# Kernel tuning notes

Hardware: AMD Instinct MI355X
Metric: run time of the kernel (lower is better)

Reference implementation:

```python
import jax, jax.numpy as jnp
import numpy as np

B, T, H, W, C = 4, 8, 64, 64, 256
WS = (2, 8, 8)        # window size (t,h,w); T,H,W chosen divisible -> no padding path
SS = (1, 4, 4)        # shift = window//2 (use_shift=True)
NH = 8
HD = C // NH
HID = int(C * 2.0)    # mlp_ratio=2.0
N = WS[0] * WS[1] * WS[2]          # 128 tokens per window
SCALE = HD ** -0.5
RPB_SIZE = (2 * WS[0] - 1) * (2 * WS[1] - 1) * (2 * WS[2] - 1)  # 675


def _rel_index(ws):
    coords = np.stack(np.meshgrid(np.arange(ws[0]), np.arange(ws[1]), np.arange(ws[2]), indexing='ij'))
    cf = coords.reshape(3, -1)
    rc = (cf[:, :, None] - cf[:, None, :]).transpose(1, 2, 0).astype(np.int64)
    rc[..., 0] += ws[0] - 1
    rc[..., 1] += ws[1] - 1
    rc[..., 2] += ws[2] - 1
    rc[..., 0] *= (2 * ws[1] - 1) * (2 * ws[2] - 1)
    rc[..., 1] *= 2 * ws[2] - 1
    return rc.sum(-1)  # [N, N]

REL_IDX = jnp.asarray(_rel_index(WS))


def _attn_mask(t, h, w, ws, ss):
    img = np.zeros((t, h, w), np.float32)
    cnt = 0
    for ts in (slice(0, -ws[0]), slice(-ws[0], -ss[0]), slice(-ss[0], None)):
        for hs in (slice(0, -ws[1]), slice(-ws[1], -ss[1]), slice(-ss[1], None)):
            for wsl in (slice(0, -ws[2]), slice(-ws[2], -ss[2]), slice(-ss[2], None)):
                img[ts, hs, wsl] = cnt
                cnt += 1
    mw = img.reshape(t // ws[0], ws[0], h // ws[1], ws[1], w // ws[2], ws[2])
    mw = mw.transpose(0, 2, 4, 1, 3, 5).reshape(-1, ws[0] * ws[1] * ws[2])  # [nW, N]
    am = mw[:, None, :] - mw[:, :, None]
    return np.where(am != 0, -100.0, 0.0).astype(np.float32)  # [nW, N, N]

ATTN_MASK = jnp.asarray(_attn_mask(T, H, W, WS, SS))


def layernorm(x, g, b):
    m = x.mean(-1, keepdims=True)
    v = x.var(-1, keepdims=True)
    return (x - m) / jnp.sqrt(v + 1e-5) * g + b


def win_part(x):
    # [B,T,H,W,C] -> [B*nW, N, C]
    x = x.reshape(B, T // WS[0], WS[0], H // WS[1], WS[1], W // WS[2], WS[2], C)
    return x.transpose(0, 1, 3, 5, 2, 4, 6, 7).reshape(-1, N, C)


def win_rev(w):
    x = w.reshape(B, T // WS[0], H // WS[1], W // WS[2], WS[0], WS[1], WS[2], C)
    return x.transpose(0, 1, 4, 2, 5, 3, 6, 7).reshape(B, T, H, W, C)


def win_attn(xw, rpb, qkv_w, qkv_b, proj_w, proj_b, mask):
    Bw = xw.shape[0]
    qkv = (xw @ qkv_w + qkv_b).reshape(Bw, N, 3, NH, HD).transpose(2, 0, 3, 1, 4)
    q, k, v = qkv[0] * SCALE, qkv[1], qkv[2]          # [Bw, NH, N, HD]
    a = jnp.einsum('bhnd,bhmd->bhnm', q, k)
    bias = rpb[REL_IDX.reshape(-1)].reshape(N, N, NH).transpose(2, 0, 1)
    a = a + bias[None]
    if mask is not None:
        nW = mask.shape[0]
        a = (a.reshape(Bw // nW, nW, NH, N, N) + mask[None, :, None]).reshape(Bw, NH, N, N)
    a = jax.nn.softmax(a, -1)
    o = jnp.einsum('bhnm,bhmd->bhnd', a, v).transpose(0, 2, 1, 3).reshape(Bw, N, C)
    return o @ proj_w + proj_b


def mlp(x, w1, b1, w2, b2):
    return jax.nn.gelu(x @ w1 + b1, approximate=False) @ w2 + b2


def setup_inputs():
    key = jax.random.key(0)
    ks = jax.random.split(key, 16)
    s = 0.02
    inp = {
        'x': jax.random.normal(ks[0], (B, T, H, W, C), jnp.float32),
        'rpb1': jax.random.normal(ks[1], (RPB_SIZE, NH), jnp.float32) * s,
        'qkv_w1': jax.random.normal(ks[2], (C, 3 * C), jnp.float32) * s,
        'qkv_b1': jnp.zeros((3 * C,), jnp.float32),
        'proj_w1': jax.random.normal(ks[3], (C, C), jnp.float32) * s,
        'proj_b1': jnp.zeros((C,), jnp.float32),
        'rpb2': jax.random.normal(ks[4], (RPB_SIZE, NH), jnp.float32) * s,
        'qkv_w2': jax.random.normal(ks[5], (C, 3 * C), jnp.float32) * s,
        'qkv_b2': jnp.zeros((3 * C,), jnp.float32),
        'proj_w2': jax.random.normal(ks[6], (C, C), jnp.float32) * s,
        'proj_b2': jnp.zeros((C,), jnp.float32),
        'g1': jnp.ones((C,), jnp.float32), 'be1': jnp.zeros((C,), jnp.float32),
        'g2': jnp.ones((C,), jnp.float32), 'be2': jnp.zeros((C,), jnp.float32),
        'g3': jnp.ones((C,), jnp.float32), 'be3': jnp.zeros((C,), jnp.float32),
        'g4': jnp.ones((C,), jnp.float32), 'be4': jnp.zeros((C,), jnp.float32),
        'm1w1': jax.random.normal(ks[7], (C, HID), jnp.float32) * s,
        'm1b1': jnp.zeros((HID,), jnp.float32),
        'm1w2': jax.random.normal(ks[8], (HID, C), jnp.float32) * s,
        'm1b2': jnp.zeros((C,), jnp.float32),
        'm2w1': jax.random.normal(ks[9], (C, HID), jnp.float32) * s,
        'm2b1': jnp.zeros((HID,), jnp.float32),
        'm2w2': jax.random.normal(ks[10], (HID, C), jnp.float32) * s,
        'm2b2': jnp.zeros((C,), jnp.float32),
    }
    return inp


def reference(x, rpb1, qkv_w1, qkv_b1, proj_w1, proj_b1,
              rpb2, qkv_w2, qkv_b2, proj_w2, proj_b2,
              g1, be1, g2, be2, g3, be3, g4, be4,
              m1w1, m1b1, m1w2, m1b2, m2w1, m2b1, m2w2, m2b2):
    # block 1: plain window attention (no shift)
    shortcut = x
    xw = win_part(layernorm(x, g1, be1))
    aw = win_attn(xw, rpb1, qkv_w1, qkv_b1, proj_w1, proj_b1, None)
    x = shortcut + win_rev(aw)
    x = x + mlp(layernorm(x, g2, be2), m1w1, m1b1, m1w2, m1b2)
    # block 2: shifted window attention with mask
    shortcut = x
    xn = layernorm(x, g3, be3)
    sx = jnp.roll(xn, (-SS[0], -SS[1], -SS[2]), axis=(1, 2, 3))
    aw = win_attn(win_part(sx), rpb2, qkv_w2, qkv_b2, proj_w2, proj_b2, ATTN_MASK)
    x = shortcut + jnp.roll(win_rev(aw), SS, axis=(1, 2, 3))
    x = x + mlp(layernorm(x, g4, be4), m2w1, m2b1, m2w2, m2b2)
    return x
```

## Files before the change

kernel.cpp:

```cpp
#include <hip/hip_runtime.h>
#include <stdint.h>

typedef __bf16 bf16_t;
using bf16x8 = __attribute__((ext_vector_type(8))) __bf16;
using f32x4  = __attribute__((ext_vector_type(4))) float;

#define DEVINL __device__ __forceinline__

DEVINL void gload_lds16(const bf16_t* g, char* l) {
  __builtin_amdgcn_global_load_lds(
      (const __attribute__((address_space(1))) void*)g,
      (__attribute__((address_space(3))) void*)l, 16, 0, 0);
}

__global__ void conv_w(const float* __restrict__ w, bf16_t* __restrict__ wt,
                       int kshift, int N, int total) {
  int i = blockIdx.x * 256 + threadIdx.x;
  if (i >= total) return;
  int n = i >> kshift, k = i & ((1 << kshift) - 1);
  wt[i] = (bf16_t)w[(size_t)k * N + n];
}

__global__ void build_bias(const float* __restrict__ rpb, float* __restrict__ tab) {
  int idx = blockIdx.x * 256 + threadIdx.x;
  int n = idx >> 7, m = idx & 127;
  int it1 = n >> 6, ih1 = (n >> 3) & 7, iw1 = n & 7;
  int it2 = m >> 6, ih2 = (m >> 3) & 7, iw2 = m & 7;
  int ridx = (it1 - it2 + 1) * 225 + (ih1 - ih2 + 7) * 15 + (iw1 - iw2 + 7);
#pragma unroll
  for (int h = 0; h < 8; ++h)
    tab[(h << 14) + idx] = rpb[ridx * 8 + h];
}

__global__ __launch_bounds__(256)
void ln_kernel(const float* __restrict__ x, const float* __restrict__ g,
               const float* __restrict__ b, bf16_t* __restrict__ out) {
  int row = blockIdx.x * 4 + (threadIdx.x >> 6);
  int lane = threadIdx.x & 63;
  float4 v = *((const float4*)(x + (size_t)row * 256) + lane);
  float s = v.x + v.y + v.z + v.w;
#pragma unroll
  for (int m = 1; m < 64; m <<= 1) s += __shfl_xor(s, m);
  float mean = s * 0.00390625f;
  float dx = v.x - mean, dy = v.y - mean, dz = v.z - mean, dw = v.w - mean;
  float s2 = dx * dx + dy * dy + dz * dz + dw * dw;
#pragma unroll
  for (int m = 1; m < 64; m <<= 1) s2 += __shfl_xor(s2, m);
  float rstd = rsqrtf(s2 * 0.00390625f + 1e-5f);
  float4 gv = *((const float4*)g + lane);
  float4 bv = *((const float4*)b + lane);
  union { bf16_t h[4]; uint2 u; } pk;
  pk.h[0] = (bf16_t)(dx * rstd * gv.x + bv.x);
  pk.h[1] = (bf16_t)(dy * rstd * gv.y + bv.y);
  pk.h[2] = (bf16_t)(dz * rstd * gv.z + bv.z);
  pk.h[3] = (bf16_t)(dw * rstd * gv.w + bv.w);
  *(uint2*)(out + (size_t)row * 256 + lane * 4) = pk.u;
}

template <int EPI>
__global__ __launch_bounds__(256, 2)
void gemm_bt(const bf16_t* __restrict__ A, const bf16_t* __restrict__ Bt,
             const float* __restrict__ bias, const float* __restrict__ resid,
             void* __restrict__ outp, int M, int N, int K, float qscale, int qcols) {
  __shared__ __align__(16) char ldsA[16384];
  __shared__ __align__(16) char ldsB[16384];
  const int tid = threadIdx.x;
  const int lane = tid & 63, wid = tid >> 6;
  const int l15 = lane & 15, l4 = lane >> 4;
  const int tn = blockIdx.x, tm = blockIdx.y;
  const int wm = wid >> 1, wn = wid & 1;

  f32x4 acc[4][4] = {};
  const int nK = K >> 6;
  const size_t arow0 = (size_t)(tm * 128) * K;

  for (int kt = 0; kt < nK; ++kt) {
    const int kb = kt * 64;
#pragma unroll
    for (int i = 0; i < 4; ++i) {
      int c = i * 256 + tid;
      int row = c >> 3, slot = c & 7;
      int ss = slot ^ (row & 7);
      gload_lds16(A + arow0 + (size_t)row * K + kb + ss * 8,
                  ldsA + (i * 256 + wid * 64) * 16);
      gload_lds16(Bt + (size_t)(tn * 128 + row) * K + kb + ss * 8,
                  ldsB + (i * 256 + wid * 64) * 16);
    }
    __syncthreads();
    bf16x8 af[4][2], bfr[4][2];
#pragma unroll
    for (int mi = 0; mi < 4; ++mi) {
      int row = wm * 64 + mi * 16 + l15;
      int sw = (row & 7) << 4;
#pragma unroll
      for (int kk = 0; kk < 2; ++kk)
        af[mi][kk] = *(const bf16x8*)(ldsA + row * 128 + ((kk * 64 + l4 * 16) ^ sw));
    }
#pragma unroll
    for (int ni = 0; ni < 4; ++ni) {
      int row = wn * 64 + ni * 16 + l15;
      int sw = (row & 7) << 4;
#pragma unroll
      for (int kk = 0; kk < 2; ++kk)
        bfr[ni][kk] = *(const bf16x8*)(ldsB + row * 128 + ((kk * 64 + l4 * 16) ^ sw));
    }
#pragma unroll
    for (int kk = 0; kk < 2; ++kk)
#pragma unroll
      for (int mi = 0; mi < 4; ++mi)
#pragma unroll
        for (int ni = 0; ni < 4; ++ni)
          acc[mi][ni] = __builtin_amdgcn_mfma_f32_16x16x32_bf16(
              af[mi][kk], bfr[ni][kk], acc[mi][ni], 0, 0, 0);
    __syncthreads();
  }

#pragma unroll
  for (int mi = 0; mi < 4; ++mi) {
#pragma unroll
    for (int ni = 0; ni < 4; ++ni) {
      int col = tn * 128 + wn * 64 + ni * 16 + l15;
      float bv = bias[col];
#pragma unroll
      for (int v = 0; v < 4; ++v) {
        int row = tm * 128 + wm * 64 + mi * 16 + l4 * 4 + v;
        float val = acc[mi][ni][v] + bv;
        size_t idx = (size_t)row * N + col;
        if constexpr (EPI == 0) {
          if (col < qcols) val *= qscale;
          ((bf16_t*)outp)[idx] = (bf16_t)val;
        } else if constexpr (EPI == 1) {
          ((float*)outp)[idx] = resid[idx] + val;
        } else {
          ((bf16_t*)outp)[idx] =
              (bf16_t)(0.5f * val * (1.0f + erff(val * 0.7071067811865475f)));
        }
      }
    }
  }
}

template <bool SHIFTED>
__global__ __launch_bounds__(256, 2)
void attn_kernel(const bf16_t* __restrict__ qkv, const float* __restrict__ btab,
                 bf16_t* __restrict__ o) {
  __shared__ int tok_s[128];
  __shared__ int rid_s[128];
  __shared__ __align__(16) char VtL[8192];
  __shared__ __align__(16) char PL[32768];

  const int tid = threadIdx.x, lane = tid & 63, wid = tid >> 6;
  const int l15 = lane & 15, l4 = lane >> 4;
  const int blk = blockIdx.x;
  const int head = blk & 7;
  const int win = blk >> 3;
  const int b = win >> 8, rem = win & 255;
  const int tw = rem >> 6, hw = (rem >> 3) & 7, ww = rem & 7;

  if (tid < 128) {
    int it = tid >> 6, ih = (tid >> 3) & 7, iw = tid & 7;
    int pt = tw * 2 + it, ph = hw * 8 + ih, pw = ww * 8 + iw;
    int t = pt, h = ph, w = pw;
    if (SHIFTED) {
      t = (pt + 1) & 7; h = (ph + 4) & 63; w = (pw + 4) & 63;
      int rt = pt < 6 ? 0 : (pt < 7 ? 1 : 2);
      int rh = ph < 56 ? 0 : (ph < 60 ? 1 : 2);
      int rw2 = pw < 56 ? 0 : (pw < 60 ? 1 : 2);
      rid_s[tid] = rt * 9 + rh * 3 + rw2;
    }
    tok_s[tid] = ((b * 8 + t) << 12) + (h << 6) + w;
  }
  __syncthreads();

  const int hoff = head << 5;
#pragma unroll
  for (int i = 0; i < 2; ++i) {
    int c = i * 256 + tid;
    int tok = c >> 2, dc = c & 3;
    bf16x8 vv = *(const bf16x8*)(qkv + (size_t)tok_s[tok] * 768 + 512 + hoff + dc * 8);
#pragma unroll
    for (int j = 0; j < 8; ++j) {
      int d = dc * 8 + j;
      *(bf16_t*)(VtL + d * 256 + ((tok * 2) ^ ((d & 7) << 4))) = vv[j];
    }
  }

  bf16x8 qf[2], kf[8];
#pragma unroll
  for (int mi = 0; mi < 2; ++mi) {
    int tok = tok_s[wid * 32 + mi * 16 + l15];
    qf[mi] = *(const bf16x8*)(qkv + (size_t)tok * 768 + hoff + l4 * 8);
  }
#pragma unroll
  for (int ni = 0; ni < 8; ++ni) {
    int tok = tok_s[ni * 16 + l15];
    kf[ni] = *(const bf16x8*)(qkv + (size_t)tok * 768 + 256 + hoff + l4 * 8);
  }
  const f32x4 zz = {0.f, 0.f, 0.f, 0.f};
  f32x4 s[2][8];
#pragma unroll
  for (int mi = 0; mi < 2; ++mi)
#pragma unroll
    for (int ni = 0; ni < 8; ++ni)
      s[mi][ni] = __builtin_amdgcn_mfma_f32_16x16x32_bf16(qf[mi], kf[ni], zz, 0, 0, 0);

  const float* bt = btab + (head << 14);
#pragma unroll
  for (int mi = 0; mi < 2; ++mi) {
#pragma unroll
    for (int v = 0; v < 4; ++v) {
      int row = wid * 32 + mi * 16 + l4 * 4 + v;
      float mx = -1e30f;
#pragma unroll
      for (int ni = 0; ni < 8; ++ni) {
        int col = ni * 16 + l15;
        float xx = s[mi][ni][v] + bt[(row << 7) + col];
        if (SHIFTED) { if (rid_s[row] != rid_s[col]) xx -= 100.f; }
        s[mi][ni][v] = xx;
        mx = fmaxf(mx, xx);
      }
#pragma unroll
      for (int d = 1; d < 16; d <<= 1) mx = fmaxf(mx, __shfl_xor(mx, d));
      float sum = 0.f;
#pragma unroll
      for (int ni = 0; ni < 8; ++ni) {
        float e = __expf(s[mi][ni][v] - mx);
        s[mi][ni][v] = e;
        sum += e;
      }
#pragma unroll
      for (int d = 1; d < 16; d <<= 1) sum += __shfl_xor(sum, d);
      float inv = 1.0f / sum;
      int sw = (row & 7) << 4;
#pragma unroll
      for (int ni = 0; ni < 8; ++ni) {
        int col = ni * 16 + l15;
        *(bf16_t*)(PL + row * 256 + ((col * 2) ^ sw)) = (bf16_t)(s[mi][ni][v] * inv);
      }
    }
  }
  __syncthreads();

  f32x4 oacc[2][2] = {};
#pragma unroll
  for (int kk = 0; kk < 4; ++kk) {
    bf16x8 pf[2], vf[2];
#pragma unroll
    for (int mi = 0; mi < 2; ++mi) {
      int row = wid * 32 + mi * 16 + l15;
      pf[mi] = *(const bf16x8*)(PL + row * 256 + ((kk * 64 + l4 * 16) ^ ((row & 7) << 4)));
    }
#pragma unroll
    for (int nj = 0; nj < 2; ++nj) {
      int d = nj * 16 + l15;
      vf[nj] = *(const bf16x8*)(VtL + d * 256 + ((kk * 64 + l4 * 16) ^ ((d & 7) << 4)));
    }
#pragma unroll
    for (int mi = 0; mi < 2; ++mi)
#pragma unroll
      for (int nj = 0; nj < 2; ++nj)
        oacc[mi][nj] = __builtin_amdgcn_mfma_f32_16x16x32_bf16(pf[mi], vf[nj], oacc[mi][nj], 0, 0, 0);
  }
#pragma unroll
  for (int mi = 0; mi < 2; ++mi)
#pragma unroll
    for (int v = 0; v < 4; ++v) {
      int tok = tok_s[wid * 32 + mi * 16 + l4 * 4 + v];
#pragma unroll
      for (int nj = 0; nj < 2; ++nj) {
        int col = nj * 16 + l15;
        o[(size_t)tok * 256 + hoff + col] = (bf16_t)(oacc[mi][nj][v]);
      }
    }
}

extern "C" void kernel_launch(void* const* d_in, const int* in_sizes, int n_in,
                              void* d_out, int out_size, void* d_ws, size_t ws_size,
                              hipStream_t stream) {
  const float* x       = (const float*)d_in[0];
  const float* rpb1    = (const float*)d_in[1];
  const float* qkv_w1  = (const float*)d_in[2];
  const float* qkv_b1  = (const float*)d_in[3];
  const float* proj_w1 = (const float*)d_in[4];
  const float* proj_b1 = (const float*)d_in[5];
  const float* rpb2    = (const float*)d_in[6];
  const float* qkv_w2  = (const float*)d_in[7];
  const float* qkv_b2  = (const float*)d_in[8];
  const float* proj_w2 = (const float*)d_in[9];
  const float* proj_b2 = (const float*)d_in[10];
  const float* g1  = (const float*)d_in[11];
  const float* be1 = (const float*)d_in[12];
  const float* g2  = (const float*)d_in[13];
  const float* be2 = (const float*)d_in[14];
  const float* g3  = (const float*)d_in[15];
  const float* be3 = (const float*)d_in[16];
  const float* g4  = (const float*)d_in[17];
  const float* be4 = (const float*)d_in[18];
  const float* m1w1 = (const float*)d_in[19];
  const float* m1b1 = (const float*)d_in[20];
  const float* m1w2 = (const float*)d_in[21];
  const float* m1b2 = (const float*)d_in[22];
  const float* m2w1 = (const float*)d_in[23];
  const float* m2b1 = (const float*)d_in[24];
  const float* m2w2 = (const float*)d_in[25];
  const float* m2b2 = (const float*)d_in[26];
  float* out = (float*)d_out;

  char* ws = (char*)d_ws;
  bf16_t* qkvb = (bf16_t*)ws;
  bf16_t* xn   = (bf16_t*)(ws + 201326592ull);
  bf16_t* wts  = (bf16_t*)(ws + 268435456ull);
  float* btab1 = (float*)(ws + 270532608ull);
  float* btab2 = btab1 + 131072;

  bf16_t* qw1t = wts;
  bf16_t* pw1t = wts + 196608;
  bf16_t* a1t  = wts + 262144;
  bf16_t* a2t  = wts + 393216;
  bf16_t* qw2t = wts + 524288;
  bf16_t* pw2t = wts + 720896;
  bf16_t* c1t  = wts + 786432;
  bf16_t* c2t  = wts + 917504;

  conv_w<<<768, 256, 0, stream>>>(qkv_w1, qw1t, 8, 768, 196608);
  conv_w<<<256, 256, 0, stream>>>(proj_w1, pw1t, 8, 256, 65536);
  conv_w<<<512, 256, 0, stream>>>(m1w1, a1t, 8, 512, 131072);
  conv_w<<<512, 256, 0, stream>>>(m1w2, a2t, 9, 256, 131072);
  conv_w<<<768, 256, 0, stream>>>(qkv_w2, qw2t, 8, 768, 196608);
  conv_w<<<256, 256, 0, stream>>>(proj_w2, pw2t, 8, 256, 65536);
  conv_w<<<512, 256, 0, stream>>>(m2w1, c1t, 8, 512, 131072);
  conv_w<<<512, 256, 0, stream>>>(m2w2, c2t, 9, 256, 131072);
  build_bias<<<64, 256, 0, stream>>>(rpb1, btab1);
  build_bias<<<64, 256, 0, stream>>>(rpb2, btab2);

  const float SC = 0.17677669529663687f;
  const int M = 131072;

  ln_kernel<<<32768, 256, 0, stream>>>(x, g1, be1, xn);
  gemm_bt<0><<<dim3(6, 1024), 256, 0, stream>>>(xn, qw1t, qkv_b1, nullptr, qkvb, M, 768, 256, SC, 256);
  attn_kernel<false><<<8192, 256, 0, stream>>>(qkvb, btab1, xn);
  gemm_bt<1><<<dim3(2, 1024), 256, 0, stream>>>(xn, pw1t, proj_b1, x, out, M, 256, 256, 1.f, 0);
  ln_kernel<<<32768, 256, 0, stream>>>(out, g2, be2, xn);
  gemm_bt<2><<<dim3(4, 1024), 256, 0, stream>>>(xn, a1t, m1b1, nullptr, qkvb, M, 512, 256, 1.f, 0);
  gemm_bt<1><<<dim3(2, 1024), 256, 0, stream>>>(qkvb, a2t, m1b2, out, out, M, 256, 512, 1.f, 0);

  ln_kernel<<<32768, 256, 0, stream>>>(out, g3, be3, xn);
  gemm_bt<0><<<dim3(6, 1024), 256, 0, stream>>>(xn, qw2t, qkv_b2, nullptr, qkvb, M, 768, 256, SC, 256);
  attn_kernel<true><<<8192, 256, 0, stream>>>(qkvb, btab2, xn);
  gemm_bt<1><<<dim3(2, 1024), 256, 0, stream>>>(xn, pw2t, proj_b2, out, out, M, 256, 256, 1.f, 0);
  ln_kernel<<<32768, 256, 0, stream>>>(out, g4, be4, xn);
  gemm_bt<2><<<dim3(4, 1024), 256, 0, stream>>>(xn, c1t, m2b1, nullptr, qkvb, M, 512, 256, 1.f, 0);
  gemm_bt<1><<<dim3(2, 1024), 256, 0, stream>>>(qkvb, c2t, m2b2, out, out, M, 256, 512, 1.f, 0);
}
```

Baseline: 1.256 ms.

## Transpose attention score MFMA, fold bias+mask into bf16 accumulator init

Rewrites the attention kernel to compute S^T (K as A operand, Q as B), which puts each query's scores in one lane column. Row max/sum then need only two cross-lane shuffles, and P and O can be written with packed 8-byte stores. The relative position bias is precomputed in bf16, with the shifted-window mask folded into 8 per-category tables, and loaded directly as the MFMA accumulator init. This removes the per-element bias add and mask compare. Occupancy hint is raised to 3 blocks per SM; bias is rounded to bf16, a small precision change.

```diff
diff --git a/kernel.cpp b/kernel.cpp
--- a/kernel.cpp
+++ b/kernel.cpp
@@ -11,6 +11,13 @@
   __builtin_amdgcn_global_load_lds(
       (const __attribute__((address_space(1))) void*)g,
       (__attribute__((address_space(3))) void*)l, 16, 0, 0);
+}
+
+DEVINL uint2 pack4(float a, float b, float c, float d) {
+  union { bf16_t h[4]; uint2 u; } pk;
+  pk.h[0] = (bf16_t)a; pk.h[1] = (bf16_t)b;
+  pk.h[2] = (bf16_t)c; pk.h[3] = (bf16_t)d;
+  return pk.u;
 }
 
 __global__ void conv_w(const float* __restrict__ w, bf16_t* __restrict__ wt,
@@ -21,7 +28,7 @@
   wt[i] = (bf16_t)w[(size_t)k * N + n];
 }
 
-__global__ void build_bias(const float* __restrict__ rpb, float* __restrict__ tab) {
+__global__ void build_bias1(const float* __restrict__ rpb, bf16_t* __restrict__ tab) {
   int idx = blockIdx.x * 256 + threadIdx.x;
   int n = idx >> 7, m = idx & 127;
   int it1 = n >> 6, ih1 = (n >> 3) & 7, iw1 = n & 7;
@@ -29,7 +36,27 @@
   int ridx = (it1 - it2 + 1) * 225 + (ih1 - ih2 + 7) * 15 + (iw1 - iw2 + 7);
 #pragma unroll
   for (int h = 0; h < 8; ++h)
-    tab[(h << 14) + idx] = rpb[ridx * 8 + h];
+    tab[(h << 14) + idx] = (bf16_t)rpb[ridx * 8 + h];
+}
+
+__global__ void build_bias2(const float* __restrict__ rpb, bf16_t* __restrict__ tab) {
+  int idx = blockIdx.x * 256 + threadIdx.x;
+  int cat = blockIdx.y;
+  int ct = cat >> 2, ch = (cat >> 1) & 1, cw = cat & 1;
+  int n = idx >> 7, m = idx & 127;
+  int it1 = n >> 6, ih1 = (n >> 3) & 7, iw1 = n & 7;
+  int it2 = m >> 6, ih2 = (m >> 3) & 7, iw2 = m & 7;
+  int rt1 = ct ? (it1 == 0 ? 1 : 2) : 0;
+  int rh1 = ch ? (ih1 < 4 ? 1 : 2) : 0;
+  int rw1 = cw ? (iw1 < 4 ? 1 : 2) : 0;
+  int rt2 = ct ? (it2 == 0 ? 1 : 2) : 0;
+  int rh2 = ch ? (ih2 < 4 ? 1 : 2) : 0;
+  int rw2 = cw ? (iw2 < 4 ? 1 : 2) : 0;
+  float msk = (rt1 != rt2 || rh1 != rh2 || rw1 != rw2) ? -100.f : 0.f;
+  int ridx = (it1 - it2 + 1) * 225 + (ih1 - ih2 + 7) * 15 + (iw1 - iw2 + 7);
+#pragma unroll
+  for (int h = 0; h < 8; ++h)
+    tab[(size_t)((cat * 8 + h) << 14) + idx] = (bf16_t)(rpb[ridx * 8 + h] + msk);
 }
 
 __global__ __launch_bounds__(256)
@@ -141,13 +168,12 @@
 }
 
 template <bool SHIFTED>
-__global__ __launch_bounds__(256, 2)
-void attn_kernel(const bf16_t* __restrict__ qkv, const float* __restrict__ btab,
+__global__ __launch_bounds__(256, 3)
+void attn_kernel(const bf16_t* __restrict__ qkv, const bf16_t* __restrict__ btab,
                  bf16_t* __restrict__ o) {
   __shared__ int tok_s[128];
-  __shared__ int rid_s[128];
   __shared__ __align__(16) char VtL[8192];
-  __shared__ __align__(16) char PL[32768];
+  __shared__ __align__(16) char PLt[32768];
 
   const int tid = threadIdx.x, lane = tid & 63, wid = tid >> 6;
   const int l15 = lane & 15, l4 = lane >> 4;
@@ -163,14 +189,18 @@
     int t = pt, h = ph, w = pw;
     if (SHIFTED) {
       t = (pt + 1) & 7; h = (ph + 4) & 63; w = (pw + 4) & 63;
-      int rt = pt < 6 ? 0 : (pt < 7 ? 1 : 2);
-      int rh = ph < 56 ? 0 : (ph < 60 ? 1 : 2);
-      int rw2 = pw < 56 ? 0 : (pw < 60 ? 1 : 2);
-      rid_s[tid] = rt * 9 + rh * 3 + rw2;
     }
     tok_s[tid] = ((b * 8 + t) << 12) + (h << 6) + w;
   }
   __syncthreads();
+
+  const bf16_t* bt;
+  if (SHIFTED) {
+    int cat = ((tw == 3) ? 4 : 0) | ((hw == 7) ? 2 : 0) | ((ww == 7) ? 1 : 0);
+    bt = btab + ((size_t)(cat * 8 + head) << 14);
+  } else {
+    bt = btab + ((size_t)head << 14);
+  }
 
   const int hoff = head << 5;
 #pragma unroll
@@ -185,58 +215,61 @@
     }
   }
 
-  bf16x8 qf[2], kf[8];
-#pragma unroll
-  for (int mi = 0; mi < 2; ++mi) {
-    int tok = tok_s[wid * 32 + mi * 16 + l15];
-    qf[mi] = *(const bf16x8*)(qkv + (size_t)tok * 768 + hoff + l4 * 8);
-  }
-#pragma unroll
-  for (int ni = 0; ni < 8; ++ni) {
-    int tok = tok_s[ni * 16 + l15];
-    kf[ni] = *(const bf16x8*)(qkv + (size_t)tok * 768 + 256 + hoff + l4 * 8);
-  }
-  const f32x4 zz = {0.f, 0.f, 0.f, 0.f};
-  f32x4 s[2][8];
-#pragma unroll
-  for (int mi = 0; mi < 2; ++mi)
-#pragma unroll
-    for (int ni = 0; ni < 8; ++ni)
-      s[mi][ni] = __builtin_amdgcn_mfma_f32_16x16x32_bf16(qf[mi], kf[ni], zz, 0, 0, 0);
-
-  const float* bt = btab + (head << 14);
-#pragma unroll
-  for (int mi = 0; mi < 2; ++mi) {
-#pragma unroll
-    for (int v = 0; v < 4; ++v) {
-      int row = wid * 32 + mi * 16 + l4 * 4 + v;
-      float mx = -1e30f;
-#pragma unroll
-      for (int ni = 0; ni < 8; ++ni) {
-        int col = ni * 16 + l15;
-        float xx = s[mi][ni][v] + bt[(row << 7) + col];
-        if (SHIFTED) { if (rid_s[row] != rid_s[col]) xx -= 100.f; }
-        s[mi][ni][v] = xx;
-        mx = fmaxf(mx, xx);
-      }
-#pragma unroll
-      for (int d = 1; d < 16; d <<= 1) mx = fmaxf(mx, __shfl_xor(mx, d));
-      float sum = 0.f;
-#pragma unroll
-      for (int ni = 0; ni < 8; ++ni) {
-        float e = __expf(s[mi][ni][v] - mx);
-        s[mi][ni][v] = e;
+  bf16x8 kf[8], qf[2];
+#pragma unroll
+  for (int ki = 0; ki < 8; ++ki) {
+    int tok = tok_s[ki * 16 + l15];
+    kf[ki] = *(const bf16x8*)(qkv + (size_t)tok * 768 + 256 + hoff + l4 * 8);
+  }
+#pragma unroll
+  for (int qi = 0; qi < 2; ++qi) {
+    int tok = tok_s[wid * 32 + qi * 16 + l15];
+    qf[qi] = *(const bf16x8*)(qkv + (size_t)tok * 768 + hoff + l4 * 8);
+  }
+
+  f32x4 st[8][2];
+#pragma unroll
+  for (int ki = 0; ki < 8; ++ki)
+#pragma unroll
+    for (int qi = 0; qi < 2; ++qi) {
+      int q = wid * 32 + qi * 16 + l15;
+      uint2 bu = *(const uint2*)(bt + (q << 7) + ki * 16 + l4 * 4);
+      f32x4 c;
+      c[0] = __uint_as_float(bu.x << 16);
+      c[1] = __uint_as_float(bu.x & 0xffff0000u);
+      c[2] = __uint_as_float(bu.y << 16);
+      c[3] = __uint_as_float(bu.y & 0xffff0000u);
+      st[ki][qi] = __builtin_amdgcn_mfma_f32_16x16x32_bf16(kf[ki], qf[qi], c, 0, 0, 0);
+    }
+
+#pragma unroll
+  for (int qi = 0; qi < 2; ++qi) {
+    float mx = -1e30f;
+#pragma unroll
+    for (int ki = 0; ki < 8; ++ki)
+#pragma unroll
+      for (int v = 0; v < 4; ++v) mx = fmaxf(mx, st[ki][qi][v]);
+    mx = fmaxf(mx, __shfl_xor(mx, 16));
+    mx = fmaxf(mx, __shfl_xor(mx, 32));
+    float sum = 0.f;
+#pragma unroll
+    for (int ki = 0; ki < 8; ++ki)
+#pragma unroll
+      for (int v = 0; v < 4; ++v) {
+        float e = __expf(st[ki][qi][v] - mx);
+        st[ki][qi][v] = e;
         sum += e;
       }
-#pragma unroll
-      for (int d = 1; d < 16; d <<= 1) sum += __shfl_xor(sum, d);
-      float inv = 1.0f / sum;
-      int sw = (row & 7) << 4;
-#pragma unroll
-      for (int ni = 0; ni < 8; ++ni) {
-        int col = ni * 16 + l15;
-        *(bf16_t*)(PL + row * 256 + ((col * 2) ^ sw)) = (bf16_t)(s[mi][ni][v] * inv);
-      }
+    sum += __shfl_xor(sum, 16);
+    sum += __shfl_xor(sum, 32);
+    float inv = 1.0f / sum;
+    int q = wid * 32 + qi * 16 + l15;
+    int sw = (q & 7) << 5;
+#pragma unroll
+    for (int ki = 0; ki < 8; ++ki) {
+      uint2 pk = pack4(st[ki][qi][0] * inv, st[ki][qi][1] * inv,
+                       st[ki][qi][2] * inv, st[ki][qi][3] * inv);
+      *(uint2*)(PLt + q * 256 + ((ki * 32 + l4 * 8) ^ sw)) = pk;
     }
   }
   __syncthreads();
@@ -244,34 +277,34 @@
   f32x4 oacc[2][2] = {};
 #pragma unroll
   for (int kk = 0; kk < 4; ++kk) {
-    bf16x8 pf[2], vf[2];
-#pragma unroll
-    for (int mi = 0; mi < 2; ++mi) {
-      int row = wid * 32 + mi * 16 + l15;
-      pf[mi] = *(const bf16x8*)(PL + row * 256 + ((kk * 64 + l4 * 16) ^ ((row & 7) << 4)));
-    }
-#pragma unroll
-    for (int nj = 0; nj < 2; ++nj) {
-      int d = nj * 16 + l15;
-      vf[nj] = *(const bf16x8*)(VtL + d * 256 + ((kk * 64 + l4 * 16) ^ ((d & 7) << 4)));
-    }
-#pragma unroll
-    for (int mi = 0; mi < 2; ++mi)
-#pragma unroll
-      for (int nj = 0; nj < 2; ++nj)
-        oacc[mi][nj] = __builtin_amdgcn_mfma_f32_16x16x32_bf16(pf[mi], vf[nj], oacc[mi][nj], 0, 0, 0);
-  }
-#pragma unroll
-  for (int mi = 0; mi < 2; ++mi)
-#pragma unroll
-    for (int v = 0; v < 4; ++v) {
-      int tok = tok_s[wid * 32 + mi * 16 + l4 * 4 + v];
-#pragma unroll
-      for (int nj = 0; nj < 2; ++nj) {
-        int col = nj * 16 + l15;
-        o[(size_t)tok * 256 + hoff + col] = (bf16_t)(oacc[mi][nj][v]);
-      }
-    }
+    bf16x8 vf[2], pf[2];
+#pragma unroll
+    for (int dj = 0; dj < 2; ++dj) {
+      int d = dj * 16 + l15;
+      vf[dj] = *(const bf16x8*)(VtL + d * 256 + ((kk * 64 + l4 * 16) ^ ((d & 7) << 4)));
+    }
+#pragma unroll
+    for (int qi = 0; qi < 2; ++qi) {
+      int q = wid * 32 + qi * 16 + l15;
+      pf[qi] = *(const bf16x8*)(PLt + q * 256 + ((kk * 64 + l4 * 16) ^ ((q & 7) << 5)));
+    }
+#pragma unroll
+    for (int dj = 0; dj < 2; ++dj)
+#pragma unroll
+      for (int qi = 0; qi < 2; ++qi)
+        oacc[dj][qi] = __builtin_amdgcn_mfma_f32_16x16x32_bf16(vf[dj], pf[qi], oacc[dj][qi], 0, 0, 0);
+  }
+
+#pragma unroll
+  for (int qi = 0; qi < 2; ++qi) {
+    int tok = tok_s[wid * 32 + qi * 16 + l15];
+#pragma unroll
+    for (int dj = 0; dj < 2; ++dj) {
+      uint2 pk = pack4(oacc[dj][qi][0], oacc[dj][qi][1],
+                       oacc[dj][qi][2], oacc[dj][qi][3]);
+      *(uint2*)(o + (size_t)tok * 256 + hoff + dj * 16 + l4 * 4) = pk;
+    }
+  }
 }
 
 extern "C" void kernel_launch(void* const* d_in, const int* in_sizes, int n_in,
@@ -310,8 +343,8 @@
   bf16_t* qkvb = (bf16_t*)ws;
   bf16_t* xn   = (bf16_t*)(ws + 201326592ull);
   bf16_t* wts  = (bf16_t*)(ws + 268435456ull);
-  float* btab1 = (float*)(ws + 270532608ull);
-  float* btab2 = btab1 + 131072;
+  bf16_t* btab1 = (bf16_t*)(ws + 270532608ull);
+  bf16_t* btab2 = (bf16_t*)(ws + 270794752ull);
 
   bf16_t* qw1t = wts;
   bf16_t* pw1t = wts + 196608;
@@ -330,8 +363,8 @@
   conv_w<<<256, 256, 0, stream>>>(proj_w2, pw2t, 8, 256, 65536);
   conv_w<<<512, 256, 0, stream>>>(m2w1, c1t, 8, 512, 131072);
   conv_w<<<512, 256, 0, stream>>>(m2w2, c2t, 9, 256, 131072);
-  build_bias<<<64, 256, 0, stream>>>(rpb1, btab1);
-  build_bias<<<64, 256, 0, stream>>>(rpb2, btab2);
+  build_bias1<<<64, 256, 0, stream>>>(rpb1, btab1);
+  build_bias2<<<dim3(64, 8), 256, 0, stream>>>(rpb2, btab2);
 
   const float SC = 0.17677669529663687f;
   const int M = 131072;
```

New measurement: 1.281 ms. Within noise of the previous version (+2.0%).
